# Performance work log

Measured on AMD Instinct MI355X. Metric: run time of the kernel, lower is better.

Reference implementation:

```python
import jax, jax.numpy as jnp
import numpy as np

COS_EPS = 1e-6      # torch CosineSimilarity eps
NORM_EPS = 1e-12    # F.normalize default eps
NUM_HEADS = 4
TOPK = 5


def setup_inputs() -> dict:
    key = jax.random.key(0)
    ks = jax.random.split(key, 12)
    B, S, D_in, D = 32, 256, 768, 1024
    N = 50000
    sc = 0.02
    return {
        "hidden": jax.random.normal(ks[0], (B, S, D_in), jnp.float32),
        "table": jax.random.normal(ks[1], (N, D), jnp.float32),
        "fc1_w": jax.random.normal(ks[2], (D, D_in), jnp.float32) * sc,
        "fc1_b": jax.random.normal(ks[3], (D,), jnp.float32) * sc,
        "q_w": jax.random.normal(ks[4], (D, D), jnp.float32) * sc,
        "q_b": jax.random.normal(ks[5], (D,), jnp.float32) * sc,
        "k_w": jax.random.normal(ks[6], (D, D), jnp.float32) * sc,
        "k_b": jax.random.normal(ks[7], (D,), jnp.float32) * sc,
        "v_w": jax.random.normal(ks[8], (D, D), jnp.float32) * sc,
        "v_b": jax.random.normal(ks[9], (D,), jnp.float32) * sc,
        "out_w": jax.random.normal(ks[10], (D, D), jnp.float32) * sc,
        "out_b": jax.random.normal(ks[11], (D,), jnp.float32) * sc,
    }


def reference(hidden, table, fc1_w, fc1_b, q_w, q_b, k_w, k_b, v_w, v_b, out_w, out_b):
    B, S, _ = hidden.shape
    D = fc1_w.shape[0]
    H = NUM_HEADS
    hd = D // H

    # fc1 over last BERT hidden states: [B,S,1024]
    x = jnp.einsum("bsi,di->bsd", hidden, fc1_w) + fc1_b

    # ---- per-sample retrieval (vectorized over batch) ----
    m = jnp.mean(x, axis=1)                       # [B,D] mean over seq
    tn = jnp.linalg.norm(table, axis=1)           # [N]
    mn = jnp.linalg.norm(m, axis=1)               # [B]
    sim = (m @ table.T) / (jnp.maximum(mn, COS_EPS)[:, None]
                           * jnp.maximum(tn, COS_EPS)[None, :])  # [B,N]
    best = jnp.argmax(sim, axis=1)                # [B] top-1 cosine match

    tab_n = table / jnp.maximum(tn, NORM_EPS)[:, None]  # L2-normalized table
    sel = tab_n[best]                             # [B,D]
    # squared euclidean distance, expanded form (avoids [B,N,D] intermediate)
    d2 = (jnp.sum(sel * sel, axis=1)[:, None]
          - 2.0 * (sel @ tab_n.T)
          + jnp.sum(tab_n * tab_n, axis=1)[None, :])  # [B,N]
    _, idx = jax.lax.top_k(-d2, TOPK)             # 5 smallest distances
    targets = table[idx]                          # [B,5,D] (unnormalized rows)

    # ---- torch.nn.MultiheadAttention(query=targets, key=x, value=x) ----
    q = (jnp.einsum("bqd,ed->bqe", targets, q_w) + q_b).reshape(B, TOPK, H, hd)
    k = (jnp.einsum("bsd,ed->bse", x, k_w) + k_b).reshape(B, S, H, hd)
    v = (jnp.einsum("bsd,ed->bse", x, v_w) + v_b).reshape(B, S, H, hd)
    scores = jnp.einsum("bqhd,bkhd->bhqk", q, k) / jnp.sqrt(jnp.asarray(hd, x.dtype))
    attn = jax.nn.softmax(scores, axis=-1)        # [B,H,5,S]
    o = jnp.einsum("bhqk,bkhd->bqhd", attn, v).reshape(B, TOPK, D)
    attn_out = jnp.einsum("bqe,de->bqd", o, out_w) + out_b  # [B,5,D]

    return jnp.sum(attn_out, axis=1)              # [B,D]
```

## Files before the change

kernel.cpp:

```cpp
#include <hip/hip_runtime.h>
#include <stdint.h>

typedef short bf16x8 __attribute__((ext_vector_type(8)));
typedef float f32x4 __attribute__((ext_vector_type(4)));

#define NROWS 50000
#define BATCH 32
#define SEQ 256
#define DIN 768
#define DMODEL 1024
#define NTOPK 5
#define DOTS_BLOCKS 782
#define CHUNKF 64
#define NCHUNK (DMODEL / CHUNKF)

__device__ inline unsigned short f2bf(float f) {
  union { float f; unsigned u; } x; x.f = f;
  unsigned u = x.u;
  unsigned r = u + 0x7fffu + ((u >> 16) & 1u);
  return (unsigned short)(r >> 16);
}
__device__ inline float bf2f(unsigned short h) {
  union { unsigned u; float f; } x; x.u = ((unsigned)h) << 16; return x.f;
}
__device__ inline ushort4 cvt_hi4(float4 f) {
  ushort4 h; h.x = f2bf(f.x); h.y = f2bf(f.y); h.z = f2bf(f.z); h.w = f2bf(f.w); return h;
}
__device__ inline ushort4 cvt_lo4(float4 f, ushort4 h) {
  ushort4 l;
  l.x = f2bf(f.x - bf2f(h.x)); l.y = f2bf(f.y - bf2f(h.y));
  l.z = f2bf(f.z - bf2f(h.z)); l.w = f2bf(f.w - bf2f(h.w));
  return l;
}

__device__ __forceinline__ void gl_lds16(const void* g, void* l) {
  __builtin_amdgcn_global_load_lds(
      (const __attribute__((address_space(1))) unsigned int*)g,
      (__attribute__((address_space(3))) unsigned int*)l, 16, 0, 0);
}

__global__ void k_f32_to_bf16(const float* __restrict__ in, unsigned short* __restrict__ out, int n) {
  int i = (blockIdx.x * blockDim.x + threadIdx.x) * 4;
  int stride = gridDim.x * blockDim.x * 4;
  for (; i < n; i += stride) {
    float4 f = *(const float4*)(in + i);
    ushort4 o;
    o.x = f2bf(f.x); o.y = f2bf(f.y); o.z = f2bf(f.z); o.w = f2bf(f.w);
    *(ushort4*)(out + i) = o;
  }
}

__global__ void k_f32_to_bf16_3(const float* __restrict__ i0, unsigned short* __restrict__ o0, int n0,
                                const float* __restrict__ i1, unsigned short* __restrict__ o1, int n1,
                                const float* __restrict__ i2, unsigned short* __restrict__ o2, int n2) {
  int base = (blockIdx.x * blockDim.x + threadIdx.x) * 4;
  int stride = gridDim.x * blockDim.x * 4;
  for (int i = base; i < n0; i += stride) {
    float4 f = *(const float4*)(i0 + i);
    ushort4 o; o.x = f2bf(f.x); o.y = f2bf(f.y); o.z = f2bf(f.z); o.w = f2bf(f.w);
    *(ushort4*)(o0 + i) = o;
  }
  for (int i = base; i < n1; i += stride) {
    float4 f = *(const float4*)(i1 + i);
    ushort4 o; o.x = f2bf(f.x); o.y = f2bf(f.y); o.z = f2bf(f.z); o.w = f2bf(f.w);
    *(ushort4*)(o1 + i) = o;
  }
  for (int i = base; i < n2; i += stride) {
    float4 f = *(const float4*)(i2 + i);
    ushort4 o; o.x = f2bf(f.x); o.y = f2bf(f.y); o.z = f2bf(f.z); o.w = f2bf(f.w);
    *(ushort4*)(o2 + i) = o;
  }
}

__global__ void k_split_q(const float* __restrict__ v, unsigned short* __restrict__ qhi,
                          unsigned short* __restrict__ qlo) {
  int b = blockIdx.x;
  int e0 = threadIdx.x * 4;
  float4 f = *(const float4*)(v + (size_t)b * DMODEL + e0);
  ushort4 h = cvt_hi4(f);
  ushort4 l = cvt_lo4(f, h);
  *(ushort4*)(qhi + (size_t)b * DMODEL + e0) = h;
  *(ushort4*)(qlo + (size_t)b * DMODEL + e0) = l;
}

__global__ void k_mean_part(const float* __restrict__ hidden, float* __restrict__ hpart) {
  int b = blockIdx.x >> 3, tc = blockIdx.x & 7;
  int i = threadIdx.x;
  const float* p = hidden + ((size_t)b * SEQ + tc * 32) * DIN + i;
  float s = 0.f;
  #pragma unroll 4
  for (int t = 0; t < 32; ++t) s += p[t * DIN];
  hpart[((size_t)tc * 32 + b) * DIN + i] = s;
}
__global__ void k_mean_reduce(const float* __restrict__ hpart, float* __restrict__ hm) {
  int b = blockIdx.x;
  int i = threadIdx.x;
  float s = 0.f;
  #pragma unroll
  for (int tc = 0; tc < 8; ++tc) s += hpart[((size_t)tc * 32 + b) * DIN + i];
  hm[b * DIN + i] = s * (1.0f / SEQ);
}

__global__ void k_sgemm_wt(const float* __restrict__ A, const float* __restrict__ W,
                           const float* __restrict__ bias, float* __restrict__ C,
                           int M, int N, int K, float beta) {
  __shared__ float A_l[32][65];
  __shared__ float W_l[64][65];
  int tid = threadIdx.x;
  int tx = tid & 63, ty = tid >> 6;
  int n0 = blockIdx.x * 64, m0 = blockIdx.y * 32;
  float acc[8] = {0.f,0.f,0.f,0.f,0.f,0.f,0.f,0.f};
  for (int k0 = 0; k0 < K; k0 += 64) {
    #pragma unroll
    for (int i = 0; i < 8; ++i) {
      int idx = tid + 256 * i; int r = idx >> 6, c = idx & 63;
      A_l[r][c] = A[(size_t)(m0 + r) * K + k0 + c];
    }
    #pragma unroll
    for (int i = 0; i < 16; ++i) {
      int idx = tid + 256 * i; int r = idx >> 6, c = idx & 63;
      W_l[r][c] = W[(size_t)(n0 + r) * K + k0 + c];
    }
    __syncthreads();
    for (int kk = 0; kk < 64; ++kk) {
      float wv = W_l[tx][kk];
      #pragma unroll
      for (int r = 0; r < 8; ++r) acc[r] += A_l[ty * 8 + r][kk] * wv;
    }
    __syncthreads();
  }
  float bv = bias[n0 + tx] * beta;
  #pragma unroll
  for (int r = 0; r < 8; ++r) C[(size_t)(m0 + ty * 8 + r) * N + n0 + tx] = acc[r] + bv;
}

__global__ __launch_bounds__(256) void k_bf16_gemm(const unsigned short* __restrict__ A,
    const unsigned short* __restrict__ W, const float* __restrict__ bias,
    unsigned short* __restrict__ C, int M, int N, int K) {
  __shared__ unsigned short As[128][32];
  __shared__ unsigned short Ws[128][32];
  int tid = threadIdx.x;
  int wave = tid >> 6, lane = tid & 63;
  int wr = wave >> 1, wc = wave & 1;
  int bm = blockIdx.y * 128, bn = blockIdx.x * 128;
  int srow = lane >> 2;
  int scol = (lane & 3) * 8;
  f32x4 acc[4][4] = {};
  for (int k0 = 0; k0 < K; k0 += 32) {
    #pragma unroll
    for (int j = 0; j < 2; ++j) {
      int r0 = wave * 32 + j * 16;
      gl_lds16(A + (size_t)(bm + r0 + srow) * K + k0 + scol, &As[r0][0]);
      gl_lds16(W + (size_t)(bn + r0 + srow) * K + k0 + scol, &Ws[r0][0]);
    }
    __syncthreads();
    bf16x8 af[4], bfr[4];
    #pragma unroll
    for (int mi = 0; mi < 4; ++mi)
      af[mi] = *(const bf16x8*)(&As[wr * 64 + mi * 16 + (lane & 15)][(lane >> 4) * 8]);
    #pragma unroll
    for (int ni = 0; ni < 4; ++ni)
      bfr[ni] = *(const bf16x8*)(&Ws[wc * 64 + ni * 16 + (lane & 15)][(lane >> 4) * 8]);
    #pragma unroll
    for (int mi = 0; mi < 4; ++mi)
      #pragma unroll
      for (int ni = 0; ni < 4; ++ni)
        acc[mi][ni] = __builtin_amdgcn_mfma_f32_16x16x32_bf16(af[mi], bfr[ni], acc[mi][ni], 0, 0, 0);
    __syncthreads();
  }
  #pragma unroll
  for (int ni = 0; ni < 4; ++ni) {
    int col = bn + wc * 64 + ni * 16 + (lane & 15);
    float bv = bias[col];
    #pragma unroll
    for (int mi = 0; mi < 4; ++mi) {
      #pragma unroll
      for (int j = 0; j < 4; ++j) {
        int row = bm + wr * 64 + mi * 16 + (lane >> 4) * 4 + j;
        C[(size_t)row * N + col] = f2bf(acc[mi][ni][j] + bv);
      }
    }
  }
}

__global__ __launch_bounds__(256, 4) void k_dots(const float* __restrict__ table,
    const unsigned short* __restrict__ qhi, const unsigned short* __restrict__ qlo,
    float* __restrict__ norm2g, float* __restrict__ candv, int* __restrict__ candi,
    int pass1, float eps) {
  __shared__ unsigned short As_hi[2][64 * 64];
  __shared__ unsigned short As_lo[2][64 * 64];
  __shared__ float npart[64][4];
  __shared__ float iv_lds[64];
  float* dot_lds = (float*)&As_hi[0][0];

  int tid = threadIdx.x;
  int wave = tid >> 6, lane = tid & 63;
  int rbase = blockIdx.x * 64;

  int r = tid >> 2;
  int q4 = tid & 3;
  int grow = rbase + r; if (grow >= NROWS) grow = NROWS - 1;
  const float* gsrc = table + (size_t)grow * DMODEL + q4 * 16;
  int wslot0 = ((q4 * 2) ^ (r & 7)) * 8;
  int wslot1 = ((q4 * 2 + 1) ^ (r & 7)) * 8;
  int wbase = r * 64;

  int abase = (wave * 16 + (lane & 15)) * 64;
  int al7 = lane & 7;
  const unsigned short* qh0 = qhi + (size_t)(lane & 15) * DMODEL + (lane >> 4) * 8;
  const unsigned short* qh1 = qh0 + 16 * DMODEL;
  const unsigned short* ql0 = qlo + (size_t)(lane & 15) * DMODEL + (lane >> 4) * 8;
  const unsigned short* ql1 = ql0 + 16 * DMODEL;

  float accn = 0.f;
  f32x4 acc0 = {}, acc1 = {};
  float4 f0, f1, f2, f3;

  auto LOAD = [&](int k0) {
    f0 = *(const float4*)(gsrc + k0);
    f1 = *(const float4*)(gsrc + k0 + 4);
    f2 = *(const float4*)(gsrc + k0 + 8);
    f3 = *(const float4*)(gsrc + k0 + 12);
  };
  auto WRITE = [&](int buf) {
    ushort4 h0 = cvt_hi4(f0), h1 = cvt_hi4(f1), h2 = cvt_hi4(f2), h3 = cvt_hi4(f3);
    ushort4 l0 = cvt_lo4(f0, h0), l1 = cvt_lo4(f1, h1), l2 = cvt_lo4(f2, h2), l3 = cvt_lo4(f3, h3);
    accn += f0.x*f0.x + f0.y*f0.y + f0.z*f0.z + f0.w*f0.w
          + f1.x*f1.x + f1.y*f1.y + f1.z*f1.z + f1.w*f1.w
          + f2.x*f2.x + f2.y*f2.y + f2.z*f2.z + f2.w*f2.w
          + f3.x*f3.x + f3.y*f3.y + f3.z*f3.z + f3.w*f3.w;
    *(ushort4*)&As_hi[buf][wbase + wslot0]     = h0;
    *(ushort4*)&As_hi[buf][wbase + wslot0 + 4] = h1;
    *(ushort4*)&As_hi[buf][wbase + wslot1]     = h2;
    *(ushort4*)&As_hi[buf][wbase + wslot1 + 4] = h3;
    *(ushort4*)&As_lo[buf][wbase + wslot0]     = l0;
    *(ushort4*)&As_lo[buf][wbase + wslot0 + 4] = l1;
    *(ushort4*)&As_lo[buf][wbase + wslot1]     = l2;
    *(ushort4*)&As_lo[buf][wbase + wslot1 + 4] = l3;
  };

  LOAD(0);
  for (int ch = 0; ch < NCHUNK; ++ch) {
    int buf = ch & 1;
    int k0 = ch * CHUNKF;
    WRITE(buf);
    if (ch + 1 < NCHUNK) LOAD(k0 + CHUNKF);
    #pragma unroll
    for (int kk = 0; kk < 2; ++kk) {
      int s = ((kk * 4 + (lane >> 4)) ^ al7) * 8;
      bf16x8 ah = *(const bf16x8*)&As_hi[buf][abase + s];
      bf16x8 al = *(const bf16x8*)&As_lo[buf][abase + s];
      int qoff = k0 + kk * 32;
      bf16x8 bh0 = *(const bf16x8*)(qh0 + qoff);
      bf16x8 bh1 = *(const bf16x8*)(qh1 + qoff);
      bf16x8 bl0 = *(const bf16x8*)(ql0 + qoff);
      bf16x8 bl1 = *(const bf16x8*)(ql1 + qoff);
      acc0 = __builtin_amdgcn_mfma_f32_16x16x32_bf16(ah, bh0, acc0, 0, 0, 0);
      acc1 = __builtin_amdgcn_mfma_f32_16x16x32_bf16(ah, bh1, acc1, 0, 0, 0);
      acc0 = __builtin_amdgcn_mfma_f32_16x16x32_bf16(ah, bl0, acc0, 0, 0, 0);
      acc1 = __builtin_amdgcn_mfma_f32_16x16x32_bf16(ah, bl1, acc1, 0, 0, 0);
      acc0 = __builtin_amdgcn_mfma_f32_16x16x32_bf16(al, bh0, acc0, 0, 0, 0);
      acc1 = __builtin_amdgcn_mfma_f32_16x16x32_bf16(al, bh1, acc1, 0, 0, 0);
    }
  }

  npart[r][q4] = accn;
  __syncthreads();
  if (tid < 64) {
    int rw = rbase + tid;
    int rc = rw < NROWS ? rw : NROWS - 1;
    float n2;
    if (pass1) {
      n2 = npart[tid][0] + npart[tid][1] + npart[tid][2] + npart[tid][3];
      if (rw < NROWS) norm2g[rw] = n2;
    } else {
      n2 = norm2g[rc];
    }
    iv_lds[tid] = 1.0f / fmaxf(sqrtf(n2), eps);
  }
  __syncthreads();
  #pragma unroll
  for (int j = 0; j < 4; ++j) {
    int row = wave * 16 + (lane >> 4) * 4 + j;
    float iv = iv_lds[row];
    dot_lds[(0 * 16 + (lane & 15)) * 66 + row] = acc0[j] * iv;
    dot_lds[(1 * 16 + (lane & 15)) * 66 + row] = acc1[j] * iv;
  }
  __syncthreads();

  if (tid < 32) {
    float tv[5]; int ti[5];
    #pragma unroll
    for (int j = 0; j < 5; ++j) { tv[j] = -3.4e38f; ti[j] = 0x7fffffff; }
    for (int rr = 0; rr < 64; ++rr) {
      int rw = rbase + rr;
      if (rw >= NROWS) break;
      float v = dot_lds[tid * 66 + rr];
      if (v > tv[4] || (v == tv[4] && rw < ti[4])) {
        tv[4] = v; ti[4] = rw;
        #pragma unroll
        for (int j = 4; j > 0; --j) {
          bool sw = (tv[j] > tv[j-1]) || (tv[j] == tv[j-1] && ti[j] < ti[j-1]);
          if (sw) {
            float fv = tv[j]; tv[j] = tv[j-1]; tv[j-1] = fv;
            int ivx = ti[j]; ti[j] = ti[j-1]; ti[j-1] = ivx;
          }
        }
      }
    }
    #pragma unroll
    for (int j = 0; j < 5; ++j) {
      candv[((size_t)blockIdx.x * 32 + tid) * 5 + j] = tv[j];
      candi[((size_t)blockIdx.x * 32 + tid) * 5 + j] = ti[j];
    }
  }
}

__global__ void k_merge(const float* __restrict__ candv, const int* __restrict__ candi,
                        int* __restrict__ out_idx, int K, int nblk) {
  int b = blockIdx.x;
  int tid = threadIdx.x;
  float tv[5]; int ti[5];
  #pragma unroll
  for (int j = 0; j < 5; ++j) { tv[j] = -3.4e38f; ti[j] = 0x7fffffff; }
  for (int blk = tid; blk < nblk; blk += 256) {
    #pragma unroll
    for (int j = 0; j < 5; ++j) {
      float v = candv[((size_t)blk * 32 + b) * 5 + j];
      int idx = candi[((size_t)blk * 32 + b) * 5 + j];
      if (v > tv[4] || (v == tv[4] && idx < ti[4])) {
        tv[4] = v; ti[4] = idx;
        #pragma unroll
        for (int jj = 4; jj > 0; --jj) {
          bool sw = (tv[jj] > tv[jj-1]) || (tv[jj] == tv[jj-1] && ti[jj] < ti[jj-1]);
          if (sw) {
            float fv = tv[jj]; tv[jj] = tv[jj-1]; tv[jj-1] = fv;
            int ivx = ti[jj]; ti[jj] = ti[jj-1]; ti[jj-1] = ivx;
          }
        }
      }
    }
  }
  __shared__ float lv[256 * 5];
  __shared__ int   li[256 * 5];
  #pragma unroll
  for (int j = 0; j < 5; ++j) { lv[tid * 5 + j] = tv[j]; li[tid * 5 + j] = ti[j]; }
  __syncthreads();
  for (int off = 128; off >= 1; off >>= 1) {
    if (tid < off) {
      float av[5], bv[5]; int ai[5], bi[5];
      #pragma unroll
      for (int j = 0; j < 5; ++j) {
        av[j] = lv[tid * 5 + j]; ai[j] = li[tid * 5 + j];
        bv[j] = lv[(tid + off) * 5 + j]; bi[j] = li[(tid + off) * 5 + j];
      }
      int pa = 0, pb = 0;
      float mv[5]; int mi[5];
      #pragma unroll
      for (int j = 0; j < 5; ++j) {
        bool ta = (av[pa] > bv[pb]) || (av[pa] == bv[pb] && ai[pa] < bi[pb]);
        if (ta) { mv[j] = av[pa]; mi[j] = ai[pa]; ++pa; }
        else    { mv[j] = bv[pb]; mi[j] = bi[pb]; ++pb; }
      }
      #pragma unroll
      for (int j = 0; j < 5; ++j) { lv[tid * 5 + j] = mv[j]; li[tid * 5 + j] = mi[j]; }
    }
    __syncthreads();
  }
  if (tid == 0) {
    for (int j = 0; j < K; ++j) out_idx[b * K + j] = li[j];
  }
}

__global__ void k_gather_sel(const float* __restrict__ table, const int* __restrict__ best,
                             float* __restrict__ sel) {
  int b = blockIdx.x, e = threadIdx.x;
  int idx = best[b];
  sel[b * DMODEL + e] = table[(size_t)idx * DMODEL + e];
}

__global__ void k_gather_targets(const float* __restrict__ table, const int* __restrict__ idx5,
                                 float* __restrict__ tg) {
  int bt = blockIdx.x, e = threadIdx.x;
  int idx = idx5[bt];
  tg[(size_t)bt * DMODEL + e] = table[(size_t)idx * DMODEL + e];
}

__global__ __launch_bounds__(256) void k_attention(const float* __restrict__ q,
    const unsigned short* __restrict__ kb, const unsigned short* __restrict__ vb,
    float* __restrict__ obuf) {
  int bt = blockIdx.x;
  int b = bt / NTOPK;
  int tid = threadIdx.x;
  __shared__ float q_l[DMODEL];
  __shared__ float sc[4][SEQ];
  #pragma unroll
  for (int j = 0; j < 4; ++j) q_l[tid + 256 * j] = q[(size_t)bt * DMODEL + tid + 256 * j];
  __syncthreads();
  {
    int s = tid;
    const unsigned short* krow = kb + ((size_t)(b * SEQ + s)) * DMODEL;
    #pragma unroll
    for (int h = 0; h < 4; ++h) {
      float d = 0.f;
      for (int dd = 0; dd < 256; dd += 8) {
        uint4 pk = *(const uint4*)(krow + h * 256 + dd);
        const unsigned short* ph = (const unsigned short*)&pk;
        #pragma unroll
        for (int j2 = 0; j2 < 8; ++j2) d += bf2f(ph[j2]) * q_l[h * 256 + dd + j2];
      }
      sc[h][s] = d * 0.0625f;
    }
  }
  __syncthreads();
  {
    int h = tid >> 6, lane = tid & 63;
    float vals[4];
    float mx = -3.4e38f;
    #pragma unroll
    for (int j = 0; j < 4; ++j) { vals[j] = sc[h][lane + 64 * j]; mx = fmaxf(mx, vals[j]); }
    #pragma unroll
    for (int o = 1; o < 64; o <<= 1) mx = fmaxf(mx, __shfl_xor(mx, o));
    float sum = 0.f;
    #pragma unroll
    for (int j = 0; j < 4; ++j) { vals[j] = expf(vals[j] - mx); sum += vals[j]; }
    #pragma unroll
    for (int o = 1; o < 64; o <<= 1) sum += __shfl_xor(sum, o);
    float rz = 1.0f / sum;
    #pragma unroll
    for (int j = 0; j < 4; ++j) sc[h][lane + 64 * j] = vals[j] * rz;
  }
  __syncthreads();
  {
    int h = tid >> 6;
    int e0 = tid * 4;
    float a0 = 0.f, a1 = 0.f, a2 = 0.f, a3 = 0.f;
    const unsigned short* vbase = vb + (size_t)(b * SEQ) * DMODEL + e0;
    for (int s = 0; s < SEQ; ++s) {
      float w = sc[h][s];
      ushort4 v4 = *(const ushort4*)(vbase + (size_t)s * DMODEL);
      a0 += w * bf2f(v4.x); a1 += w * bf2f(v4.y); a2 += w * bf2f(v4.z); a3 += w * bf2f(v4.w);
    }
    float* op = obuf + (size_t)bt * DMODEL + e0;
    op[0] = a0; op[1] = a1; op[2] = a2; op[3] = a3;
  }
}

__global__ void k_osum(const float* __restrict__ obuf, float* __restrict__ osum) {
  int g = blockIdx.x * blockDim.x + threadIdx.x;
  if (g >= BATCH * DMODEL) return;
  int b = g >> 10, e = g & 1023;
  float s = 0.f;
  #pragma unroll
  for (int t = 0; t < NTOPK; ++t) s += obuf[(size_t)(b * NTOPK + t) * DMODEL + e];
  osum[g] = s;
}

extern "C" void kernel_launch(void* const* d_in, const int* in_sizes, int n_in,
                              void* d_out, int out_size, void* d_ws, size_t ws_size,
                              hipStream_t stream) {
  const float* hidden = (const float*)d_in[0];
  const float* table  = (const float*)d_in[1];
  const float* fc1_w  = (const float*)d_in[2];
  const float* fc1_b  = (const float*)d_in[3];
  const float* q_w    = (const float*)d_in[4];
  const float* q_b    = (const float*)d_in[5];
  const float* k_w    = (const float*)d_in[6];
  const float* k_b    = (const float*)d_in[7];
  const float* v_w    = (const float*)d_in[8];
  const float* v_b    = (const float*)d_in[9];
  const float* out_w  = (const float*)d_in[10];
  const float* out_b  = (const float*)d_in[11];
  float* out = (float*)d_out;

  char* ws = (char*)d_ws;
  size_t off = 0;
  auto alloc = [&](size_t bytes) -> void* {
    void* p = ws + off;
    off += (bytes + 255) & ~(size_t)255;
    return p;
  };
  unsigned short* hid_bf  = (unsigned short*)alloc((size_t)BATCH * SEQ * DIN * 2);
  unsigned short* fc1w_bf = (unsigned short*)alloc((size_t)DMODEL * DIN * 2);
  unsigned short* kw_bf   = (unsigned short*)alloc((size_t)DMODEL * DMODEL * 2);
  unsigned short* vw_bf   = (unsigned short*)alloc((size_t)DMODEL * DMODEL * 2);
  unsigned short* x_bf    = (unsigned short*)alloc((size_t)BATCH * SEQ * DMODEL * 2);
  unsigned short* k_bf    = (unsigned short*)alloc((size_t)BATCH * SEQ * DMODEL * 2);
  unsigned short* v_bf    = (unsigned short*)alloc((size_t)BATCH * SEQ * DMODEL * 2);
  unsigned short* qhi     = (unsigned short*)alloc((size_t)BATCH * DMODEL * 2);
  unsigned short* qlo     = (unsigned short*)alloc((size_t)BATCH * DMODEL * 2);
  float* hpart   = (float*)alloc((size_t)8 * BATCH * DIN * 4);
  float* hm      = (float*)alloc((size_t)BATCH * DIN * 4);
  float* m       = (float*)alloc((size_t)BATCH * DMODEL * 4);
  float* sel     = (float*)alloc((size_t)BATCH * DMODEL * 4);
  float* norm2   = (float*)alloc((size_t)NROWS * 4);
  float* candv   = (float*)alloc((size_t)DOTS_BLOCKS * 32 * 5 * 4);
  int*   candi   = (int*)alloc((size_t)DOTS_BLOCKS * 32 * 5 * 4);
  int*   best    = (int*)alloc(BATCH * 4);
  int*   idx5    = (int*)alloc(BATCH * NTOPK * 4);
  float* targets = (float*)alloc((size_t)BATCH * NTOPK * DMODEL * 4);
  float* qbuf    = (float*)alloc((size_t)BATCH * NTOPK * DMODEL * 4);
  float* obuf    = (float*)alloc((size_t)BATCH * NTOPK * DMODEL * 4);
  float* osum    = (float*)alloc((size_t)BATCH * DMODEL * 4);
  (void)ws_size; (void)in_sizes; (void)n_in; (void)out_size;

  k_f32_to_bf16<<<2048, 256, 0, stream>>>(hidden, hid_bf, BATCH * SEQ * DIN);
  k_f32_to_bf16_3<<<1024, 256, 0, stream>>>(fc1_w, fc1w_bf, DMODEL * DIN,
                                            k_w, kw_bf, DMODEL * DMODEL,
                                            v_w, vw_bf, DMODEL * DMODEL);

  k_mean_part<<<256, 768, 0, stream>>>(hidden, hpart);
  k_mean_reduce<<<32, 768, 0, stream>>>(hpart, hm);
  k_sgemm_wt<<<dim3(16, 1), 256, 0, stream>>>(hm, fc1_w, fc1_b, m, 32, DMODEL, DIN, 1.0f);

  k_bf16_gemm<<<dim3(8, 64), 256, 0, stream>>>(hid_bf, fc1w_bf, fc1_b, x_bf, BATCH * SEQ, DMODEL, DIN);

  k_split_q<<<32, 256, 0, stream>>>(m, qhi, qlo);
  k_dots<<<DOTS_BLOCKS, 256, 0, stream>>>(table, qhi, qlo, norm2, candv, candi, 1, 1e-6f);
  k_merge<<<32, 256, 0, stream>>>(candv, candi, best, 1, DOTS_BLOCKS);
  k_gather_sel<<<32, 1024, 0, stream>>>(table, best, sel);

  k_split_q<<<32, 256, 0, stream>>>(sel, qhi, qlo);
  k_dots<<<DOTS_BLOCKS, 256, 0, stream>>>(table, qhi, qlo, norm2, candv, candi, 0, 1e-12f);
  k_merge<<<32, 256, 0, stream>>>(candv, candi, idx5, NTOPK, DOTS_BLOCKS);
  k_gather_targets<<<160, 1024, 0, stream>>>(table, idx5, targets);

  k_sgemm_wt<<<dim3(16, 5), 256, 0, stream>>>(targets, q_w, q_b, qbuf, BATCH * NTOPK, DMODEL, DMODEL, 1.0f);

  k_bf16_gemm<<<dim3(8, 64), 256, 0, stream>>>(x_bf, kw_bf, k_b, k_bf, BATCH * SEQ, DMODEL, DMODEL);
  k_bf16_gemm<<<dim3(8, 64), 256, 0, stream>>>(x_bf, vw_bf, v_b, v_bf, BATCH * SEQ, DMODEL, DMODEL);

  k_attention<<<160, 256, 0, stream>>>(qbuf, k_bf, v_bf, obuf);
  k_osum<<<128, 256, 0, stream>>>(obuf, osum);
  k_sgemm_wt<<<dim3(16, 1), 256, 0, stream>>>(osum, out_w, out_b, out, 32, DMODEL, DMODEL, 5.0f);
}
```

Before: 592.5 us.

## Split table dot kernel along K into halves with separate combine/top-k kernel

The table-scan dot kernel now launches twice as many blocks, each covering half of the feature dimension. Partial dot products and partial norms go to global memory, and a new combine kernel sums them, normalizes, and does the per-block top-5 selection. This aims to raise parallelism and occupancy on the memory-bound table scan, since 782 blocks underfill the GPU. In exchange it adds an extra launch per pass and extra global traffic for partial results. It also hoists the query operand loads ahead of the LDS write to overlap their latency.

Measured after the change: 584.2 us, median of 2. About the same (-1.4%).

```diff
diff --git a/kernel.cpp b/kernel.cpp
--- a/kernel.cpp
+++ b/kernel.cpp
@@ -10,9 +10,9 @@
 #define DIN 768
 #define DMODEL 1024
 #define NTOPK 5
-#define DOTS_BLOCKS 782
+#define DOTS_RG 782
 #define CHUNKF 64
-#define NCHUNK (DMODEL / CHUNKF)
+#define NCHUNK_HALF 8
 
 __device__ inline unsigned short f2bf(float f) {
   union { float f; unsigned u; } x; x.f = f;
@@ -185,31 +185,31 @@
 
 __global__ __launch_bounds__(256, 4) void k_dots(const float* __restrict__ table,
     const unsigned short* __restrict__ qhi, const unsigned short* __restrict__ qlo,
-    float* __restrict__ norm2g, float* __restrict__ candv, int* __restrict__ candi,
-    int pass1, float eps) {
+    float* __restrict__ normp, float* __restrict__ dotsg, int pass1) {
   __shared__ unsigned short As_hi[2][64 * 64];
   __shared__ unsigned short As_lo[2][64 * 64];
   __shared__ float npart[64][4];
-  __shared__ float iv_lds[64];
   float* dot_lds = (float*)&As_hi[0][0];
 
   int tid = threadIdx.x;
   int wave = tid >> 6, lane = tid & 63;
-  int rbase = blockIdx.x * 64;
+  int rg = blockIdx.x >> 1, half = blockIdx.x & 1;
+  int rbase = rg * 64;
+  int kbase = half * 512;
 
   int r = tid >> 2;
   int q4 = tid & 3;
   int grow = rbase + r; if (grow >= NROWS) grow = NROWS - 1;
-  const float* gsrc = table + (size_t)grow * DMODEL + q4 * 16;
+  const float* gsrc = table + (size_t)grow * DMODEL + kbase + q4 * 16;
   int wslot0 = ((q4 * 2) ^ (r & 7)) * 8;
   int wslot1 = ((q4 * 2 + 1) ^ (r & 7)) * 8;
   int wbase = r * 64;
 
   int abase = (wave * 16 + (lane & 15)) * 64;
   int al7 = lane & 7;
-  const unsigned short* qh0 = qhi + (size_t)(lane & 15) * DMODEL + (lane >> 4) * 8;
+  const unsigned short* qh0 = qhi + (size_t)(lane & 15) * DMODEL + (lane >> 4) * 8 + kbase;
   const unsigned short* qh1 = qh0 + 16 * DMODEL;
-  const unsigned short* ql0 = qlo + (size_t)(lane & 15) * DMODEL + (lane >> 4) * 8;
+  const unsigned short* ql0 = qlo + (size_t)(lane & 15) * DMODEL + (lane >> 4) * 8 + kbase;
   const unsigned short* ql1 = ql0 + 16 * DMODEL;
 
   float accn = 0.f;
@@ -240,62 +240,98 @@
   };
 
   LOAD(0);
-  for (int ch = 0; ch < NCHUNK; ++ch) {
+  for (int ch = 0; ch < NCHUNK_HALF; ++ch) {
     int buf = ch & 1;
     int k0 = ch * CHUNKF;
+    bf16x8 bh0[2], bh1[2], bl0[2], bl1[2];
+    #pragma unroll
+    for (int kk = 0; kk < 2; ++kk) {
+      int qoff = k0 + kk * 32;
+      bh0[kk] = *(const bf16x8*)(qh0 + qoff);
+      bh1[kk] = *(const bf16x8*)(qh1 + qoff);
+      bl0[kk] = *(const bf16x8*)(ql0 + qoff);
+      bl1[kk] = *(const bf16x8*)(ql1 + qoff);
+    }
     WRITE(buf);
-    if (ch + 1 < NCHUNK) LOAD(k0 + CHUNKF);
+    if (ch + 1 < NCHUNK_HALF) LOAD(k0 + CHUNKF);
     #pragma unroll
     for (int kk = 0; kk < 2; ++kk) {
       int s = ((kk * 4 + (lane >> 4)) ^ al7) * 8;
       bf16x8 ah = *(const bf16x8*)&As_hi[buf][abase + s];
       bf16x8 al = *(const bf16x8*)&As_lo[buf][abase + s];
-      int qoff = k0 + kk * 32;
-      bf16x8 bh0 = *(const bf16x8*)(qh0 + qoff);
-      bf16x8 bh1 = *(const bf16x8*)(qh1 + qoff);
-      bf16x8 bl0 = *(const bf16x8*)(ql0 + qoff);
-      bf16x8 bl1 = *(const bf16x8*)(ql1 + qoff);
-      acc0 = __builtin_amdgcn_mfma_f32_16x16x32_bf16(ah, bh0, acc0, 0, 0, 0);
-      acc1 = __builtin_amdgcn_mfma_f32_16x16x32_bf16(ah, bh1, acc1, 0, 0, 0);
-      acc0 = __builtin_amdgcn_mfma_f32_16x16x32_bf16(ah, bl0, acc0, 0, 0, 0);
-      acc1 = __builtin_amdgcn_mfma_f32_16x16x32_bf16(ah, bl1, acc1, 0, 0, 0);
-      acc0 = __builtin_amdgcn_mfma_f32_16x16x32_bf16(al, bh0, acc0, 0, 0, 0);
-      acc1 = __builtin_amdgcn_mfma_f32_16x16x32_bf16(al, bh1, acc1, 0, 0, 0);
+      acc0 = __builtin_amdgcn_mfma_f32_16x16x32_bf16(ah, bh0[kk], acc0, 0, 0, 0);
+      acc1 = __builtin_amdgcn_mfma_f32_16x16x32_bf16(ah, bh1[kk], acc1, 0, 0, 0);
+      acc0 = __builtin_amdgcn_mfma_f32_16x16x32_bf16(ah, bl0[kk], acc0, 0, 0, 0);
+      acc1 = __builtin_amdgcn_mfma_f32_16x16x32_bf16(ah, bl1[kk], acc1, 0, 0, 0);
+      acc0 = __builtin_amdgcn_mfma_f32_16x16x32_bf16(al, bh0[kk], acc0, 0, 0, 0);
+      acc1 = __builtin_amdgcn_mfma_f32_16x16x32_bf16(al, bh1[kk], acc1, 0, 0, 0);
     }
   }
 
   npart[r][q4] = accn;
   __syncthreads();
+  if (pass1 && tid < 64) {
+    int rw = rbase + tid;
+    if (rw < NROWS) {
+      float n2 = npart[tid][0] + npart[tid][1] + npart[tid][2] + npart[tid][3];
+      normp[(size_t)half * NROWS + rw] = n2;
+    }
+  }
+  #pragma unroll
+  for (int j = 0; j < 4; ++j) {
+    int row = wave * 16 + (lane >> 4) * 4 + j;
+    dot_lds[((lane & 15)) * 68 + row] = acc0[j];
+    dot_lds[(16 + (lane & 15)) * 68 + row] = acc1[j];
+  }
+  __syncthreads();
+  {
+    int b = tid >> 3, r0 = (tid & 7) * 8;
+    float* dst = dotsg + ((size_t)blockIdx.x * 32 + b) * 64 + r0;
+    float4 v0 = *(const float4*)&dot_lds[b * 68 + r0];
+    float4 v1 = *(const float4*)&dot_lds[b * 68 + r0 + 4];
+    *(float4*)dst = v0;
+    *(float4*)(dst + 4) = v1;
+  }
+}
+
+__global__ void k_comb5(const float* __restrict__ dotsg, const float* __restrict__ normp,
+                        float* __restrict__ norm2f, float* __restrict__ candv,
+                        int* __restrict__ candi, int pass1, float eps) {
+  __shared__ float sc[32 * 68];
+  __shared__ float iv_lds[64];
+  int rg = blockIdx.x;
+  int tid = threadIdx.x;
   if (tid < 64) {
-    int rw = rbase + tid;
+    int rw = rg * 64 + tid;
     int rc = rw < NROWS ? rw : NROWS - 1;
     float n2;
     if (pass1) {
-      n2 = npart[tid][0] + npart[tid][1] + npart[tid][2] + npart[tid][3];
-      if (rw < NROWS) norm2g[rw] = n2;
+      n2 = normp[rc] + normp[NROWS + rc];
+      if (rw < NROWS) norm2f[rw] = n2;
     } else {
-      n2 = norm2g[rc];
+      n2 = norm2f[rc];
     }
     iv_lds[tid] = 1.0f / fmaxf(sqrtf(n2), eps);
   }
   __syncthreads();
-  #pragma unroll
-  for (int j = 0; j < 4; ++j) {
-    int row = wave * 16 + (lane >> 4) * 4 + j;
-    float iv = iv_lds[row];
-    dot_lds[(0 * 16 + (lane & 15)) * 66 + row] = acc0[j] * iv;
-    dot_lds[(1 * 16 + (lane & 15)) * 66 + row] = acc1[j] * iv;
-  }
-  __syncthreads();
-
+  {
+    int b = tid >> 3, r0 = (tid & 7) * 8;
+    const float* p0 = dotsg + ((size_t)(rg * 2 + 0) * 32 + b) * 64 + r0;
+    const float* p1 = dotsg + ((size_t)(rg * 2 + 1) * 32 + b) * 64 + r0;
+    #pragma unroll
+    for (int i = 0; i < 8; ++i)
+      sc[b * 68 + r0 + i] = (p0[i] + p1[i]) * iv_lds[r0 + i];
+  }
+  __syncthreads();
   if (tid < 32) {
     float tv[5]; int ti[5];
     #pragma unroll
     for (int j = 0; j < 5; ++j) { tv[j] = -3.4e38f; ti[j] = 0x7fffffff; }
+    int rbase = rg * 64;
     for (int rr = 0; rr < 64; ++rr) {
       int rw = rbase + rr;
       if (rw >= NROWS) break;
-      float v = dot_lds[tid * 66 + rr];
+      float v = sc[tid * 68 + rr];
       if (v > tv[4] || (v == tv[4] && rw < ti[4])) {
         tv[4] = v; ti[4] = rw;
         #pragma unroll
@@ -310,8 +346,8 @@
     }
     #pragma unroll
     for (int j = 0; j < 5; ++j) {
-      candv[((size_t)blockIdx.x * 32 + tid) * 5 + j] = tv[j];
-      candi[((size_t)blockIdx.x * 32 + tid) * 5 + j] = ti[j];
+      candv[((size_t)rg * 32 + tid) * 5 + j] = tv[j];
+      candi[((size_t)rg * 32 + tid) * 5 + j] = ti[j];
     }
   }
 }
@@ -493,9 +529,11 @@
   float* hm      = (float*)alloc((size_t)BATCH * DIN * 4);
   float* m       = (float*)alloc((size_t)BATCH * DMODEL * 4);
   float* sel     = (float*)alloc((size_t)BATCH * DMODEL * 4);
-  float* norm2   = (float*)alloc((size_t)NROWS * 4);
-  float* candv   = (float*)alloc((size_t)DOTS_BLOCKS * 32 * 5 * 4);
-  int*   candi   = (int*)alloc((size_t)DOTS_BLOCKS * 32 * 5 * 4);
+  float* normp   = (float*)alloc((size_t)2 * NROWS * 4);
+  float* norm2f  = (float*)alloc((size_t)NROWS * 4);
+  float* dotsg   = (float*)alloc((size_t)DOTS_RG * 2 * 32 * 64 * 4);
+  float* candv   = (float*)alloc((size_t)DOTS_RG * 32 * 5 * 4);
+  int*   candi   = (int*)alloc((size_t)DOTS_RG * 32 * 5 * 4);
   int*   best    = (int*)alloc(BATCH * 4);
   int*   idx5    = (int*)alloc(BATCH * NTOPK * 4);
   float* targets = (float*)alloc((size_t)BATCH * NTOPK * DMODEL * 4);
@@ -516,13 +554,15 @@
   k_bf16_gemm<<<dim3(8, 64), 256, 0, stream>>>(hid_bf, fc1w_bf, fc1_b, x_bf, BATCH * SEQ, DMODEL, DIN);
 
   k_split_q<<<32, 256, 0, stream>>>(m, qhi, qlo);
-  k_dots<<<DOTS_BLOCKS, 256, 0, stream>>>(table, qhi, qlo, norm2, candv, candi, 1, 1e-6f);
-  k_merge<<<32, 256, 0, stream>>>(candv, candi, best, 1, DOTS_BLOCKS);
+  k_dots<<<DOTS_RG * 2, 256, 0, stream>>>(table, qhi, qlo, normp, dotsg, 1);
+  k_comb5<<<DOTS_RG, 256, 0, stream>>>(dotsg, normp, norm2f, candv, candi, 1, 1e-6f);
+  k_merge<<<32, 256, 0, stream>>>(candv, candi, best, 1, DOTS_RG);
   k_gather_sel<<<32, 1024, 0, stream>>>(table, best, sel);
 
   k_split_q<<<32, 256, 0, stream>>>(sel, qhi, qlo);
-  k_dots<<<DOTS_BLOCKS, 256, 0, stream>>>(table, qhi, qlo, norm2, candv, candi, 0, 1e-12f);
-  k_merge<<<32, 256, 0, stream>>>(candv, candi, idx5, NTOPK, DOTS_BLOCKS);
+  k_dots<<<DOTS_RG * 2, 256, 0, stream>>>(table, qhi, qlo, normp, dotsg, 0);
+  k_comb5<<<DOTS_RG, 256, 0, stream>>>(dotsg, normp, norm2f, candv, candi, 0, 1e-12f);
+  k_merge<<<32, 256, 0, stream>>>(candv, candi, idx5, NTOPK, DOTS_RG);
   k_gather_targets<<<160, 1024, 0, stream>>>(table, idx5, targets);
 
   k_sgemm_wt<<<dim3(16, 5), 256, 0, stream>>>(targets, q_w, q_b, qbuf, BATCH * NTOPK, DMODEL, DMODEL, 1.0f);
```
